# Optimization experiments

Measured on AMD Instinct MI355X. Metric: run time of the kernel, lower is better.

## Reference

```python
import jax, jax.numpy as jnp
import numpy as np

H, C = 5, 64            # attention heads, per-head channels (out_channels=conv_dim)
NEG_SLOPE = 0.2         # GATv2 leaky_relu slope
N_NODES = 50000

def setup_inputs() -> dict:
    key = jax.random.key(0)
    ks = jax.random.split(key, 10)
    N, E = N_NODES, 400000
    node_dim, edge_dim = 128, 16
    s = 0.1
    return {
        'x': jax.random.normal(ks[0], (N, node_dim), jnp.float32),
        'edge_index': jax.random.randint(ks[1], (2, E), 0, N),
        'edge_attr': jax.random.normal(ks[2], (E, edge_dim), jnp.float32),
        'W0': jax.random.normal(ks[3], (node_dim, H * C), jnp.float32) * s,
        'b0': jnp.zeros((H * C,), jnp.float32),
        'We0': jax.random.normal(ks[4], (edge_dim, H * C), jnp.float32) * s,
        'att0': jax.random.normal(ks[5], (H, C), jnp.float32) * s,
        'bias0': jnp.zeros((C,), jnp.float32),
        'W12': jax.random.normal(ks[6], (2, C, H * C), jnp.float32) * s,
        'b12': jnp.zeros((2, H * C), jnp.float32),
        'We12': jax.random.normal(ks[7], (2, edge_dim, H * C), jnp.float32) * s,
        'att12': jax.random.normal(ks[8], (2, H, C), jnp.float32) * s,
        'bias12': jnp.zeros((2, C), jnp.float32),
    }

def _add_self_loops_mean(edge_index, edge_attr, N):
    # PyG add_self_loops(fill_value='mean'): self-loop attr = mean of incoming edge attrs per dst node
    dst = edge_index[1]
    sums = jax.ops.segment_sum(edge_attr, dst, num_segments=N)
    cnt = jax.ops.segment_sum(jnp.ones((edge_attr.shape[0], 1), edge_attr.dtype), dst, num_segments=N)
    loop_attr = sums / jnp.maximum(cnt, 1.0)
    loop = jnp.arange(N, dtype=edge_index.dtype)
    ei = jnp.concatenate([edge_index, jnp.stack([loop, loop])], axis=1)
    ea = jnp.concatenate([edge_attr, loop_attr], axis=0)
    return ei, ea

def _gatv2_layer(x, src, dst, eattr, W, b, We, att, bias, N):
    h = (x @ W + b).reshape(N, H, C)                     # shared lin_l==lin_r (share_weights=True)
    e = (eattr @ We).reshape(-1, H, C)                   # lin_edge (no bias)
    s = jax.nn.leaky_relu(h[src] + h[dst] + e, NEG_SLOPE)  # [E', H, C]
    logits = jnp.einsum('ehc,hc->eh', s, att)            # [E', H]
    m = jax.ops.segment_max(logits, dst, num_segments=N)
    m = jnp.where(jnp.isfinite(m), m, 0.0)
    ex = jnp.exp(logits - m[dst])
    denom = jax.ops.segment_sum(ex, dst, num_segments=N) + 1e-16
    alpha = ex / denom[dst]                              # per-dst softmax (dropout off: eval mode)
    msg = h[src] * alpha[:, :, None]
    out = jax.ops.segment_sum(msg, dst, num_segments=N)  # [N, H, C]
    return out.mean(axis=1) + bias                       # concat=False -> head mean, then bias

def reference(x, edge_index, edge_attr, W0, b0, We0, att0, bias0, W12, b12, We12, att12, bias12):
    N = x.shape[0]
    ei, ea = _add_self_loops_mean(edge_index, edge_attr, N)
    src, dst = ei[0], ei[1]
    h = jax.nn.elu(_gatv2_layer(x, src, dst, ea, W0, b0, We0, att0, bias0, N))
    for i in range(2):
        h = jax.nn.elu(_gatv2_layer(h, src, dst, ea, W12[i], b12[i], We12[i], att12[i], bias12[i], N))
    return h  # jk_mode='last'
```

## Files before the change

### kernel.cpp

```cpp
#include <hip/hip_runtime.h>
#include <hip/hip_fp16.h>
#include <math.h>

#define NH 5
#define NC 64
#define ED 16
#define HC 320
#define HP 8

typedef _Float16 h2  __attribute__((ext_vector_type(2)));
typedef _Float16 v8h __attribute__((ext_vector_type(8)));
typedef float    v4f __attribute__((ext_vector_type(4)));

template<int ctrl, int rmask>
__device__ __forceinline__ float dpp_add(float x) {
    int y = __builtin_amdgcn_update_dpp(0, __float_as_int(x), ctrl, rmask, 0xf, true);
    return x + __int_as_float(y);
}
__device__ __forceinline__ float wave_sum_all(float x) {
    x = dpp_add<0xb1, 0xf>(x);
    x = dpp_add<0x4e, 0xf>(x);
    x = dpp_add<0x114, 0xf>(x);
    x = dpp_add<0x118, 0xf>(x);
    x = dpp_add<0x142, 0xa>(x);
    x = dpp_add<0x143, 0xc>(x);
    return __int_as_float(__builtin_amdgcn_readlane(__float_as_int(x), 63));
}


__global__ void count_kernel(const int* __restrict__ dst, int* __restrict__ cnt, int E) {
    int t = blockIdx.x * blockDim.x + threadIdx.x;
    if (t >= E) return;
    atomicAdd(&cnt[dst[t]], 1);
}

__global__ void scan_kernel(const int* __restrict__ cnt, int* __restrict__ offsets,
                            int* __restrict__ cursor, int N) {
    __shared__ int sums[1024];
    int t = threadIdx.x;
    int chunk = (N + 1023) / 1024;
    int beg = t * chunk;
    int end = min(beg + chunk, N);
    int s = 0;
    for (int i = beg; i < end; ++i) s += cnt[i] + 1;
    sums[t] = s;
    __syncthreads();
    for (int o = 1; o < 1024; o <<= 1) {
        int v = (t >= o) ? sums[t - o] : 0;
        __syncthreads();
        sums[t] += v;
        __syncthreads();
    }
    int run = (t > 0) ? sums[t - 1] : 0;
    for (int i = beg; i < end; ++i) {
        offsets[i] = run; cursor[i] = run;
        run += cnt[i] + 1;
    }
    if (t == 0) offsets[N] = sums[1023];
}

__global__ void scatter_kernel(const int* __restrict__ src, const int* __restrict__ dst,
                               int* __restrict__ cursor, int2* __restrict__ recs, int N, int E) {
    int t = blockIdx.x * blockDim.x + threadIdx.x;
    if (t >= E + N) return;
    int d, s;
    if (t < E) { d = dst[t]; s = src[t]; }
    else       { d = t - E; s = t - E; }
    int pos = atomicAdd(&cursor[d], 1);
    recs[pos] = make_int2(s, t);
}

__global__ void loop_from_csr(const int* __restrict__ offsets, const int2* __restrict__ recs,
                              const float* __restrict__ ea, float* __restrict__ loop,
                              int N, int E) {
    int t = blockIdx.x * blockDim.x + threadIdx.x;
    int n = t >> 4, k = t & 15;
    if (n >= N) return;
    int beg = offsets[n], end = offsets[n + 1];
    float s = 0.f; int c = 0;
    for (int j = beg; j < end; ++j) {
        int y = recs[j].y;
        if (y < E) { s += ea[(size_t)y * ED + k]; ++c; }
    }
    loop[(size_t)n * ED + k] = s / (float)max(c, 1);
}

__global__ void reorder_ea(const int2* __restrict__ recs, const float* __restrict__ ea,
                           const float* __restrict__ loop, h2* __restrict__ easrt,
                           int R, int E) {
    int t = blockIdx.x * blockDim.x + threadIdx.x;
    int slot = t >> 3, k2 = t & 7;
    if (slot >= R) return;
    int y = recs[slot].y;
    const float2* sp = (const float2*)((y < E) ? ea + (size_t)y * ED : loop + (size_t)(y - E) * ED);
    float2 f = sp[k2];
    h2 o; o.x = (_Float16)f.x; o.y = (_Float16)f.y;
    easrt[(size_t)slot * 8 + k2] = o;
}

__global__ void win_start_kernel(const int* __restrict__ offsets, int* __restrict__ winStart,
                                 int N, int CHw) {
    int i = blockIdx.x * blockDim.x + threadIdx.x;
    if (i >= N) return;
    atomicMin(&winStart[offsets[i] / CHw], i);
}

__global__ void transpose_w(const float* __restrict__ W, _Float16* __restrict__ Wt, int K) {
    int t = blockIdx.x * blockDim.x + threadIdx.x;
    if (t >= 320 * K) return;
    int k = t / 320, n = t % 320;
    Wt[(size_t)n * K + k] = (_Float16)W[t];
}

template<bool F32A>
__global__ __launch_bounds__(256) void gemm_mfma(const void* __restrict__ Araw,
                                                 const _Float16* __restrict__ Bt,
                                                 const float* __restrict__ bias,
                                                 _Float16* __restrict__ Cout, int M, int K) {
    __shared__ _Float16 lds[4][8][NC * HP];
    int lane = threadIdx.x & 63;
    int wave = threadIdx.x >> 6;
    int m = lane & 15, quad = lane >> 4;
    int rowBase = (blockIdx.x * 4 + wave) * 16;
    bool active = rowBase < M;

    v4f acc[20];
#pragma unroll
    for (int c = 0; c < 20; ++c) acc[c] = (v4f){0.f, 0.f, 0.f, 0.f};

    if (active) {
        for (int k0 = 0; k0 < K; k0 += 32) {
            v8h a;
            if (F32A) {
                const float* ap = (const float*)Araw + (size_t)(rowBase + m) * K + k0 + quad * 8;
                float4 f0 = *(const float4*)ap;
                float4 f1 = *(const float4*)(ap + 4);
                a[0] = (_Float16)f0.x; a[1] = (_Float16)f0.y;
                a[2] = (_Float16)f0.z; a[3] = (_Float16)f0.w;
                a[4] = (_Float16)f1.x; a[5] = (_Float16)f1.y;
                a[6] = (_Float16)f1.z; a[7] = (_Float16)f1.w;
            } else {
                a = *(const v8h*)((const _Float16*)Araw + (size_t)(rowBase + m) * K + k0 + quad * 8);
            }
#pragma unroll
            for (int c = 0; c < 20; ++c) {
                v8h b = *(const v8h*)&Bt[(size_t)(c * 16 + m) * K + k0 + quad * 8];
                acc[c] = __builtin_amdgcn_mfma_f32_16x16x32_f16(a, b, acc[c], 0, 0, 0);
            }
        }
    }
#pragma unroll
    for (int pass = 0; pass < 2; ++pass) {
        if (active && (quad >> 1) == pass) {
#pragma unroll
            for (int c = 0; c < 20; ++c) {
                int cc = c * 16 + m;
                int idx = (cc & 63) * HP + (cc >> 6);
                float bb = bias[cc];
#pragma unroll
                for (int r = 0; r < 4; ++r)
                    lds[wave][(quad & 1) * 4 + r][idx] = (_Float16)(acc[c][r] + bb);
            }
        }
        __syncthreads();
        if (active) {
#pragma unroll
            for (int rr = 0; rr < 8; ++rr) {
                v8h v = *(const v8h*)&lds[wave][rr][lane * HP];
                *(v8h*)&Cout[(size_t)(rowBase + pass * 8 + rr) * (NC * HP) + lane * HP] = v;
            }
        }
        __syncthreads();
    }
}

__global__ __launch_bounds__(256) void gat_fused(const _Float16* __restrict__ hbuf,
                                                 const int* __restrict__ offsets,
                                                 const int2* __restrict__ recs,
                                                 const h2* __restrict__ easrt,
                                                 const int* __restrict__ winStart,
                                                 const float* __restrict__ We,
                                                 const float* __restrict__ att,
                                                 const float* __restrict__ bias,
                                                 _Float16* __restrict__ outH,
                                                 float* __restrict__ outF,
                                                 int N, int R, int CHw) {
    int lane = threadIdx.x & 63;
    int w = (blockIdx.x * blockDim.x + threadIdx.x) >> 6;
    if (w * CHw >= R) return;
    int i = winStart[w];
    if (i >= N) return;
    int winEnd = w * CHw + CHw;

    h2 we2[8 * NH];
#pragma unroll
    for (int k2 = 0; k2 < 8; ++k2)
#pragma unroll
        for (int h = 0; h < NH; ++h) {
            h2 wv;
            wv.x = (_Float16)We[(2 * k2) * HC + h * NC + lane];
            wv.y = (_Float16)We[(2 * k2 + 1) * HC + h * NC + lane];
            we2[k2 * NH + h] = wv;
        }
    const float L2E = 1.4426950408889634f;
    float attc6[NH], attc4[NH];
#pragma unroll
    for (int h = 0; h < NH; ++h) {
        float a = att[h * NC + lane];
        attc6[h] = 0.6f * a * L2E;
        attc4[h] = 0.4f * a * L2E;
    }
    float bc = bias[lane];

    for (; i < N; ++i) {
        int beg = offsets[i];
        if (beg >= winEnd) break;
        int end = offsets[i + 1];

        v8h hdv = *(const v8h*)&hbuf[(size_t)i * (NC * HP) + lane * HP];
        float hd[NH];
#pragma unroll
        for (int h = 0; h < NH; ++h) hd[h] = (float)hdv[h];

        float l[NH] = {}, acc[NH] = {};
        for (int t = beg; t < end; ++t) {
            int tu = __builtin_amdgcn_readfirstlane(t);
            int src = recs[tu].x;
            const h2* ap = easrt + (size_t)tu * 8;
            h2 a[8];
#pragma unroll
            for (int k2 = 0; k2 < 8; ++k2) a[k2] = ap[k2];
            v8h hsv = *(const v8h*)&hbuf[(size_t)src * (NC * HP) + lane * HP];
            float hs[NH];
#pragma unroll
            for (int h = 0; h < NH; ++h) hs[h] = (float)hsv[h];

            float p[NH];
#pragma unroll
            for (int h = 0; h < NH; ++h) {
                float v = hs[h] + hd[h];
#pragma unroll
                for (int k2 = 0; k2 < 8; ++k2)
                    v = __builtin_amdgcn_fdot2(a[k2], we2[k2 * NH + h], v, false);
                p[h] = fmaf(fabsf(v), attc4[h], v * attc6[h]);
            }
#pragma unroll
            for (int h = 0; h < NH; ++h) {
                float pe = exp2f(wave_sum_all(p[h]));
                l[h] += pe;
                acc[h] = fmaf(pe, hs[h], acc[h]);
            }
        }
        float o = 0.f;
#pragma unroll
        for (int h = 0; h < NH; ++h) o += acc[h] / l[h];
        o = o * 0.2f + bc;
        o = o > 0.f ? o : expm1f(o);
        if (outF) outF[(size_t)i * NC + lane] = o;
        else      outH[(size_t)i * NC + lane] = (_Float16)o;
    }
}

extern "C" void kernel_launch(void* const* d_in, const int* in_sizes, int n_in,
                              void* d_out, int out_size, void* d_ws, size_t ws_size,
                              hipStream_t stream) {
    const float* x     = (const float*)d_in[0];
    const int*   ei    = (const int*)d_in[1];
    const float* ea    = (const float*)d_in[2];
    const float* W0    = (const float*)d_in[3];
    const float* b0    = (const float*)d_in[4];
    const float* We0   = (const float*)d_in[5];
    const float* att0  = (const float*)d_in[6];
    const float* bias0 = (const float*)d_in[7];
    const float* W12   = (const float*)d_in[8];
    const float* b12   = (const float*)d_in[9];
    const float* We12  = (const float*)d_in[10];
    const float* att12 = (const float*)d_in[11];
    const float* bias12= (const float*)d_in[12];

    int N = in_sizes[0] / 128;
    int E = in_sizes[1] / 2;
    int R = E + N;
    int CHw = (R + 8191) / 8192;
    int numWin = (R + CHw - 1) / CHw;
    const int* srcArr = ei;
    const int* dstArr = ei + E;

    char* ws = (char*)d_ws;
    size_t off = 0;
    auto alloc = [&](size_t bytes) -> void* {
        void* p = ws + off;
        off = (off + bytes + 255) & ~(size_t)255;
        return p;
    };
    int*      cnt     = (int*)alloc((size_t)N * 4);
    int*      offsets = (int*)alloc((size_t)(N + 1) * 4);
    int*      cursor  = (int*)alloc((size_t)N * 4);
    int2*     recs    = (int2*)alloc((size_t)R * 8);
    float*    loop    = (float*)alloc((size_t)N * ED * 4);
    _Float16* hbuf    = (_Float16*)alloc((size_t)N * NC * HP * 2);
    _Float16* acth    = (_Float16*)alloc((size_t)N * NC * 2);
    _Float16* Wth0    = (_Float16*)alloc((size_t)320 * 128 * 2);
    _Float16* Wth1    = (_Float16*)alloc((size_t)320 * 64 * 2);
    _Float16* Wth2    = (_Float16*)alloc((size_t)320 * 64 * 2);
    int*      winStart= (int*)alloc((size_t)(numWin + 1) * 4);
    h2*       easrt   = (h2*)alloc((size_t)R * 32);

    (void)hipMemsetAsync(cnt, 0, (size_t)N * 4, stream);
    (void)hipMemsetAsync(winStart, 0x7f, (size_t)(numWin + 1) * 4, stream);
    count_kernel<<<(E + 255) / 256, 256, 0, stream>>>(dstArr, cnt, E);
    scan_kernel<<<1, 1024, 0, stream>>>(cnt, offsets, cursor, N);
    scatter_kernel<<<(E + N + 255) / 256, 256, 0, stream>>>(srcArr, dstArr, cursor, recs, N, E);
    loop_from_csr<<<((size_t)N * ED + 255) / 256, 256, 0, stream>>>(offsets, recs, ea, loop, N, E);
    reorder_ea<<<((size_t)R * 8 + 255) / 256, 256, 0, stream>>>(recs, ea, loop, easrt, R, E);
    win_start_kernel<<<(N + 255) / 256, 256, 0, stream>>>(offsets, winStart, N, CHw);
    transpose_w<<<(320 * 128 + 255) / 256, 256, 0, stream>>>(W0, Wth0, 128);
    transpose_w<<<(320 * 64 + 255) / 256, 256, 0, stream>>>(W12, Wth1, 64);
    transpose_w<<<(320 * 64 + 255) / 256, 256, 0, stream>>>(W12 + 64 * HC, Wth2, 64);

    float* dout = (float*)d_out;
    int gemmBlocks = (N / 16 + 3) / 4 + 1;
    int fusedBlocks = (numWin + 3) / 4;

    const _Float16* Bts[3] = {Wth0, Wth1, Wth2};
    int Ks[3] = {128, 64, 64};
    const float* bs[3]   = {b0, b12, b12 + HC};
    const float* Wes[3]  = {We0, We12, We12 + ED * HC};
    const float* atts[3] = {att0, att12, att12 + NH * NC};
    const float* bis[3]  = {bias0, bias12, bias12 + NC};
    for (int layer = 0; layer < 3; ++layer) {
        if (layer == 0)
            gemm_mfma<true><<<gemmBlocks, 256, 0, stream>>>(x, Bts[0], bs[0], hbuf, N, Ks[0]);
        else
            gemm_mfma<false><<<gemmBlocks, 256, 0, stream>>>(acth, Bts[layer], bs[layer], hbuf, N, Ks[layer]);
        gat_fused<<<fusedBlocks, 256, 0, stream>>>(hbuf, offsets, recs, easrt, winStart,
                                                   Wes[layer], atts[layer], bis[layer],
                                                   acth, (layer == 2) ? dout : nullptr, N, R, CHw);
    }
}
```

Measured before the change: 882.9 us.

## Software-pipeline edge gathers in GAT kernel, persistent windows, fuse preprocessing kernels

The fused GAT kernel now prefetches the source index, edge attributes and source features of the next one or two edges before computing the current one. This is meant to hide gather latency. Each wave handles fixed 32-slot windows in a grid-stride loop over 2048 blocks. The self-loop is placed first in each node's CSR range, so its features double as the destination features. Preprocessing merges the loop-mean computation into the edge-attribute reorder and merges the three weight transposes into one launch, which cuts kernel launches; the cost is a redundant mean loop per self-loop lane.

```diff
diff --git a/kernel.cpp b/kernel.cpp
--- a/kernel.cpp
+++ b/kernel.cpp
@@ -7,6 +7,7 @@
 #define ED 16
 #define HC 320
 #define HP 8
+#define CH 32
 
 typedef _Float16 h2  __attribute__((ext_vector_type(2)));
 typedef _Float16 v8h __attribute__((ext_vector_type(8)));
@@ -53,63 +54,81 @@
     }
     int run = (t > 0) ? sums[t - 1] : 0;
     for (int i = beg; i < end; ++i) {
-        offsets[i] = run; cursor[i] = run;
+        offsets[i] = run; cursor[i] = run + 1;
         run += cnt[i] + 1;
     }
     if (t == 0) offsets[N] = sums[1023];
 }
 
 __global__ void scatter_kernel(const int* __restrict__ src, const int* __restrict__ dst,
-                               int* __restrict__ cursor, int2* __restrict__ recs, int N, int E) {
+                               const int* __restrict__ offsets, int* __restrict__ cursor,
+                               int2* __restrict__ recs, int N, int E) {
     int t = blockIdx.x * blockDim.x + threadIdx.x;
     if (t >= E + N) return;
-    int d, s;
-    if (t < E) { d = dst[t]; s = src[t]; }
-    else       { d = t - E; s = t - E; }
-    int pos = atomicAdd(&cursor[d], 1);
-    recs[pos] = make_int2(s, t);
-}
-
-__global__ void loop_from_csr(const int* __restrict__ offsets, const int2* __restrict__ recs,
-                              const float* __restrict__ ea, float* __restrict__ loop,
-                              int N, int E) {
-    int t = blockIdx.x * blockDim.x + threadIdx.x;
-    int n = t >> 4, k = t & 15;
-    if (n >= N) return;
-    int beg = offsets[n], end = offsets[n + 1];
-    float s = 0.f; int c = 0;
-    for (int j = beg; j < end; ++j) {
-        int y = recs[j].y;
-        if (y < E) { s += ea[(size_t)y * ED + k]; ++c; }
-    }
-    loop[(size_t)n * ED + k] = s / (float)max(c, 1);
-}
-
-__global__ void reorder_ea(const int2* __restrict__ recs, const float* __restrict__ ea,
-                           const float* __restrict__ loop, h2* __restrict__ easrt,
-                           int R, int E) {
+    if (t < E) {
+        int d = dst[t];
+        int pos = atomicAdd(&cursor[d], 1);
+        recs[pos] = make_int2(src[t], t);
+    } else {
+        int n = t - E;
+        recs[offsets[n]] = make_int2(n, t);
+    }
+}
+
+__global__ void build_easrt(const int* __restrict__ offsets, const int2* __restrict__ recs,
+                            const float* __restrict__ ea, h2* __restrict__ easrt,
+                            int R, int E) {
     int t = blockIdx.x * blockDim.x + threadIdx.x;
     int slot = t >> 3, k2 = t & 7;
     if (slot >= R) return;
     int y = recs[slot].y;
-    const float2* sp = (const float2*)((y < E) ? ea + (size_t)y * ED : loop + (size_t)(y - E) * ED);
-    float2 f = sp[k2];
-    h2 o; o.x = (_Float16)f.x; o.y = (_Float16)f.y;
+    h2 o;
+    if (y < E) {
+        float2 f = ((const float2*)(ea + (size_t)y * ED))[k2];
+        o.x = (_Float16)f.x; o.y = (_Float16)f.y;
+    } else {
+        int n = y - E;
+        int beg = offsets[n], end = offsets[n + 1];
+        float sx = 0.f, sy = 0.f; int c = 0;
+        for (int j = beg; j < end; ++j) {
+            int yj = recs[j].y;
+            if (yj < E) {
+                float2 f = ((const float2*)(ea + (size_t)yj * ED))[k2];
+                sx += f.x; sy += f.y; ++c;
+            }
+        }
+        float inv = 1.f / (float)max(c, 1);
+        o.x = (_Float16)(sx * inv); o.y = (_Float16)(sy * inv);
+    }
     easrt[(size_t)slot * 8 + k2] = o;
 }
 
-__global__ void win_start_kernel(const int* __restrict__ offsets, int* __restrict__ winStart,
-                                 int N, int CHw) {
+__global__ void win_start_kernel(const int* __restrict__ offsets, int* __restrict__ winStart, int N) {
     int i = blockIdx.x * blockDim.x + threadIdx.x;
     if (i >= N) return;
-    atomicMin(&winStart[offsets[i] / CHw], i);
-}
-
-__global__ void transpose_w(const float* __restrict__ W, _Float16* __restrict__ Wt, int K) {
+    atomicMin(&winStart[offsets[i] / CH], i);
+}
+
+__global__ void transpose_all(const float* __restrict__ W0, const float* __restrict__ W12,
+                              _Float16* __restrict__ Wt0, _Float16* __restrict__ Wt1,
+                              _Float16* __restrict__ Wt2) {
     int t = blockIdx.x * blockDim.x + threadIdx.x;
-    if (t >= 320 * K) return;
-    int k = t / 320, n = t % 320;
-    Wt[(size_t)n * K + k] = (_Float16)W[t];
+    if (t < 320 * 128) {
+        int k = t / 320, n = t % 320;
+        Wt0[(size_t)n * 128 + k] = (_Float16)W0[t];
+        return;
+    }
+    t -= 320 * 128;
+    if (t < 320 * 64) {
+        int k = t / 320, n = t % 320;
+        Wt1[(size_t)n * 64 + k] = (_Float16)W12[t];
+        return;
+    }
+    t -= 320 * 64;
+    if (t < 320 * 64) {
+        int k = t / 320, n = t % 320;
+        Wt2[(size_t)n * 64 + k] = (_Float16)W12[320 * 64 + t];
+    }
 }
 
 template<bool F32A>
@@ -184,13 +203,10 @@
                                                  const float* __restrict__ bias,
                                                  _Float16* __restrict__ outH,
                                                  float* __restrict__ outF,
-                                                 int N, int R, int CHw) {
+                                                 int N, int R, int numWin) {
     int lane = threadIdx.x & 63;
-    int w = (blockIdx.x * blockDim.x + threadIdx.x) >> 6;
-    if (w * CHw >= R) return;
-    int i = winStart[w];
-    if (i >= N) return;
-    int winEnd = w * CHw + CHw;
+    int wave = (blockIdx.x * blockDim.x + threadIdx.x) >> 6;
+    int totalWaves = (gridDim.x * blockDim.x) >> 6;
 
     h2 we2[8 * NH];
 #pragma unroll
@@ -212,52 +228,85 @@
     }
     float bc = bias[lane];
 
-    for (; i < N; ++i) {
-        int beg = offsets[i];
-        if (beg >= winEnd) break;
-        int end = offsets[i + 1];
-
-        v8h hdv = *(const v8h*)&hbuf[(size_t)i * (NC * HP) + lane * HP];
-        float hd[NH];
-#pragma unroll
-        for (int h = 0; h < NH; ++h) hd[h] = (float)hdv[h];
-
-        float l[NH] = {}, acc[NH] = {};
-        for (int t = beg; t < end; ++t) {
-            int tu = __builtin_amdgcn_readfirstlane(t);
-            int src = recs[tu].x;
-            const h2* ap = easrt + (size_t)tu * 8;
-            h2 a[8];
-#pragma unroll
-            for (int k2 = 0; k2 < 8; ++k2) a[k2] = ap[k2];
-            v8h hsv = *(const v8h*)&hbuf[(size_t)src * (NC * HP) + lane * HP];
-            float hs[NH];
-#pragma unroll
-            for (int h = 0; h < NH; ++h) hs[h] = (float)hsv[h];
-
+    for (int w = wave; w < numWin; w += totalWaves) {
+        int i = winStart[w];
+        if (i >= N) continue;
+        int winEnd = w * CH + CH;
+
+        int t = offsets[i];
+        int nodeEnd = offsets[i + 1];
+
+        int t1 = (t + 1 < R) ? t + 1 : t;
+        int s0 = recs[t].x;
+        int s1 = recs[t1].x;
+        h2 a0[8], a1[8];
+        {
+            const h2* ap0 = easrt + (size_t)t * 8;
+            const h2* ap1 = easrt + (size_t)t1 * 8;
+#pragma unroll
+            for (int k = 0; k < 8; ++k) { a0[k] = ap0[k]; a1[k] = ap1[k]; }
+        }
+        v8h hs0 = *(const v8h*)&hbuf[(size_t)s0 * (NC * HP) + lane * HP];
+
+        float hd[NH] = {}, l[NH] = {}, acc[NH] = {};
+        bool newNode = true;
+
+        while (true) {
+            int t2 = (t + 2 < R) ? t + 2 : t;
+            int s2 = recs[t2].x;
+            h2 a2[8];
+            {
+                const h2* ap2 = easrt + (size_t)t2 * 8;
+#pragma unroll
+                for (int k = 0; k < 8; ++k) a2[k] = ap2[k];
+            }
+            v8h hs1 = *(const v8h*)&hbuf[(size_t)s1 * (NC * HP) + lane * HP];
+
+            float hsf[NH];
+#pragma unroll
+            for (int h = 0; h < NH; ++h) hsf[h] = (float)hs0[h];
+            if (newNode) {
+#pragma unroll
+                for (int h = 0; h < NH; ++h) hd[h] = hsf[h];
+                newNode = false;
+            }
             float p[NH];
 #pragma unroll
             for (int h = 0; h < NH; ++h) {
-                float v = hs[h] + hd[h];
-#pragma unroll
-                for (int k2 = 0; k2 < 8; ++k2)
-                    v = __builtin_amdgcn_fdot2(a[k2], we2[k2 * NH + h], v, false);
+                float v = hsf[h] + hd[h];
+#pragma unroll
+                for (int k = 0; k < 8; ++k)
+                    v = __builtin_amdgcn_fdot2(a0[k], we2[k * NH + h], v, false);
                 p[h] = fmaf(fabsf(v), attc4[h], v * attc6[h]);
             }
 #pragma unroll
             for (int h = 0; h < NH; ++h) {
                 float pe = exp2f(wave_sum_all(p[h]));
                 l[h] += pe;
-                acc[h] = fmaf(pe, hs[h], acc[h]);
-            }
-        }
-        float o = 0.f;
-#pragma unroll
-        for (int h = 0; h < NH; ++h) o += acc[h] / l[h];
-        o = o * 0.2f + bc;
-        o = o > 0.f ? o : expm1f(o);
-        if (outF) outF[(size_t)i * NC + lane] = o;
-        else      outH[(size_t)i * NC + lane] = (_Float16)o;
+                acc[h] = fmaf(pe, hsf[h], acc[h]);
+            }
+
+            ++t;
+            if (t == nodeEnd) {
+                float o = 0.f;
+#pragma unroll
+                for (int h = 0; h < NH; ++h) o += acc[h] / l[h];
+                o = o * 0.2f + bc;
+                o = o > 0.f ? o : expm1f(o);
+                if (outF) outF[(size_t)i * NC + lane] = o;
+                else      outH[(size_t)i * NC + lane] = (_Float16)o;
+                ++i;
+                if (i >= N || nodeEnd >= winEnd) break;
+                nodeEnd = offsets[i + 1];
+#pragma unroll
+                for (int h = 0; h < NH; ++h) { l[h] = 0.f; acc[h] = 0.f; }
+                newNode = true;
+            }
+            s0 = s1; s1 = s2;
+#pragma unroll
+            for (int k = 0; k < 8; ++k) { a0[k] = a1[k]; a1[k] = a2[k]; }
+            hs0 = hs1;
+        }
     }
 }
 
@@ -281,8 +330,7 @@
     int N = in_sizes[0] / 128;
     int E = in_sizes[1] / 2;
     int R = E + N;
-    int CHw = (R + 8191) / 8192;
-    int numWin = (R + CHw - 1) / CHw;
+    int numWin = (R + CH - 1) / CH;
     const int* srcArr = ei;
     const int* dstArr = ei + E;
 
@@ -297,7 +345,6 @@
     int*      offsets = (int*)alloc((size_t)(N + 1) * 4);
     int*      cursor  = (int*)alloc((size_t)N * 4);
     int2*     recs    = (int2*)alloc((size_t)R * 8);
-    float*    loop    = (float*)alloc((size_t)N * ED * 4);
     _Float16* hbuf    = (_Float16*)alloc((size_t)N * NC * HP * 2);
     _Float16* acth    = (_Float16*)alloc((size_t)N * NC * 2);
     _Float16* Wth0    = (_Float16*)alloc((size_t)320 * 128 * 2);
@@ -310,17 +357,14 @@
     (void)hipMemsetAsync(winStart, 0x7f, (size_t)(numWin + 1) * 4, stream);
     count_kernel<<<(E + 255) / 256, 256, 0, stream>>>(dstArr, cnt, E);
     scan_kernel<<<1, 1024, 0, stream>>>(cnt, offsets, cursor, N);
-    scatter_kernel<<<(E + N + 255) / 256, 256, 0, stream>>>(srcArr, dstArr, cursor, recs, N, E);
-    loop_from_csr<<<((size_t)N * ED + 255) / 256, 256, 0, stream>>>(offsets, recs, ea, loop, N, E);
-    reorder_ea<<<((size_t)R * 8 + 255) / 256, 256, 0, stream>>>(recs, ea, loop, easrt, R, E);
-    win_start_kernel<<<(N + 255) / 256, 256, 0, stream>>>(offsets, winStart, N, CHw);
-    transpose_w<<<(320 * 128 + 255) / 256, 256, 0, stream>>>(W0, Wth0, 128);
-    transpose_w<<<(320 * 64 + 255) / 256, 256, 0, stream>>>(W12, Wth1, 64);
-    transpose_w<<<(320 * 64 + 255) / 256, 256, 0, stream>>>(W12 + 64 * HC, Wth2, 64);
+    scatter_kernel<<<(E + N + 255) / 256, 256, 0, stream>>>(srcArr, dstArr, offsets, cursor, recs, N, E);
+    build_easrt<<<((size_t)R * 8 + 255) / 256, 256, 0, stream>>>(offsets, recs, ea, easrt, R, E);
+    win_start_kernel<<<(N + 255) / 256, 256, 0, stream>>>(offsets, winStart, N);
+    transpose_all<<<(320 * 256 + 255) / 256, 256, 0, stream>>>(W0, W12, Wth0, Wth1, Wth2);
 
     float* dout = (float*)d_out;
     int gemmBlocks = (N / 16 + 3) / 4 + 1;
-    int fusedBlocks = (numWin + 3) / 4;
+    int fusedBlocks = 2048;
 
     const _Float16* Bts[3] = {Wth0, Wth1, Wth2};
     int Ks[3] = {128, 64, 64};
@@ -335,6 +379,6 @@
             gemm_mfma<false><<<gemmBlocks, 256, 0, stream>>>(acth, Bts[layer], bs[layer], hbuf, N, Ks[layer]);
         gat_fused<<<fusedBlocks, 256, 0, stream>>>(hbuf, offsets, recs, easrt, winStart,
                                                    Wes[layer], atts[layer], bis[layer],
-                                                   acth, (layer == 2) ? dout : nullptr, N, R, CHw);
-    }
-}
+                                                   acth, (layer == 2) ? dout : nullptr, N, R, numWin);
+    }
+}
```

Result: slower. 943.3 us (+6.8%).
